# Kernel optimization log

Hardware: AMD Instinct MI355X
Metric: run time of the kernel (lower is better)

The kernel has to match this reference:

```python
import jax, jax.numpy as jnp
import numpy as np

N, E, D, H, C, G, L = 100000, 1600000, 128, 4, 32, 4096, 3  # nodes, edges, h_dim, heads, head_dim, graphs, conv blocks


def setup_inputs() -> dict:
    key = jax.random.key(0)
    ks = jax.random.split(key, 24)
    s = 0.05
    w = lambda k, shape: jax.random.normal(k, shape, jnp.float32) * s
    inp = {
        "x": jax.random.normal(ks[0], (N, D), jnp.float32),
        "edge_index": jax.random.randint(ks[1], (2, E), 0, N),
        "batch": jnp.sort(jax.random.randint(ks[2], (N,), 0, G)),
        # input TransformerConv (in=D, out=C per head, H heads, beta=True)
        "in_Wq": w(ks[3], (D, D)), "in_bq": jnp.zeros((D,), jnp.float32),
        "in_Wk": w(ks[4], (D, D)), "in_bk": jnp.zeros((D,), jnp.float32),
        "in_Wv": w(ks[5], (D, D)), "in_bv": jnp.zeros((D,), jnp.float32),
        "in_Ws": w(ks[6], (D, D)), "in_bs": jnp.zeros((D,), jnp.float32),
        "in_Wbeta": w(ks[7], (3 * D,)),
        # stacked conv blocks (L of them, in=out=D)
        "blk_Wq": w(ks[8], (L, D, D)), "blk_bq": jnp.zeros((L, D), jnp.float32),
        "blk_Wk": w(ks[9], (L, D, D)), "blk_bk": jnp.zeros((L, D), jnp.float32),
        "blk_Wv": w(ks[10], (L, D, D)), "blk_bv": jnp.zeros((L, D), jnp.float32),
        "blk_Ws": w(ks[11], (L, D, D)), "blk_bs": jnp.zeros((L, D), jnp.float32),
        "blk_Wbeta": w(ks[12], (L, 3 * D)),
        # MLP head
        "W1": w(ks[13], (D, 64)), "b1": jnp.zeros((64,), jnp.float32),
        "W2": w(ks[14], (64, 32)), "b2": jnp.zeros((32,), jnp.float32),
        "W3": w(ks[15], (32, 1)), "b3": jnp.zeros((1,), jnp.float32),
    }
    return inp


def transformer_conv(x, src, dst, Wq, bq, Wk, bk, Wv, bv, Ws, bs, Wbeta):
    # PyG TransformerConv, concat=True, root_weight=True, beta=True, eval mode
    q = (x @ Wq + bq).reshape(N, H, C)
    k = (x @ Wk + bk).reshape(N, H, C)
    v = (x @ Wv + bv).reshape(N, H, C)
    # per-edge attention logits: message j=src -> i=dst
    alpha = jnp.einsum("ehc,ehc->eh", q[dst], k[src]) / jnp.sqrt(jnp.float32(C))  # [E,H]
    m = jax.ops.segment_max(alpha, dst, num_segments=N)
    m = jnp.where(jnp.isfinite(m), m, 0.0)
    e = jnp.exp(alpha - m[dst])
    denom = jax.ops.segment_sum(e, dst, num_segments=N)
    a = e / (denom[dst] + 1e-16)  # segment softmax over in-edges of dst
    msg = a[..., None] * v[src]  # [E,H,C]
    out = jax.ops.segment_sum(msg, dst, num_segments=N).reshape(N, H * C)
    x_r = x @ Ws + bs
    beta = jax.nn.sigmoid(jnp.concatenate([out, x_r, out - x_r], axis=-1) @ Wbeta)[:, None]
    return beta * x_r + (1.0 - beta) * out


def reference(x, edge_index, batch, in_Wq, in_bq, in_Wk, in_bk, in_Wv, in_bv,
              in_Ws, in_bs, in_Wbeta, blk_Wq, blk_bq, blk_Wk, blk_bk, blk_Wv,
              blk_bv, blk_Ws, blk_bs, blk_Wbeta, W1, b1, W2, b2, W3, b3):
    src, dst = edge_index[0], edge_index[1]
    h = jax.nn.relu(transformer_conv(x, src, dst, in_Wq, in_bq, in_Wk, in_bk,
                                     in_Wv, in_bv, in_Ws, in_bs, in_Wbeta))
    for l in range(L):  # dropout is identity in eval mode
        h = jax.nn.relu(transformer_conv(h, src, dst, blk_Wq[l], blk_bq[l],
                                         blk_Wk[l], blk_bk[l], blk_Wv[l], blk_bv[l],
                                         blk_Ws[l], blk_bs[l], blk_Wbeta[l]))
    # global mean pool over graphs
    sums = jax.ops.segment_sum(h, batch, num_segments=G)
    cnt = jax.ops.segment_sum(jnp.ones((N, 1), h.dtype), batch, num_segments=G)
    g = sums / jnp.maximum(cnt, 1.0)
    g = jax.nn.relu(g @ W1 + b1)
    g = jax.nn.relu(g @ W2 + b2)
    return jax.nn.sigmoid(g @ W3 + b3)
```

## Files before the change

kernel.cpp:

```cpp
#include <hip/hip_runtime.h>
#include <hip/hip_bf16.h>
#include <cstdint>

#define DH 128
#define NB 256
#define NBK 1024

typedef __attribute__((ext_vector_type(8))) short short8;
typedef __attribute__((ext_vector_type(4))) float floatx4;
typedef __attribute__((ext_vector_type(2))) float floatx2;

__device__ __forceinline__ float bflo(unsigned u) { return __uint_as_float(u << 16); }
__device__ __forceinline__ float bfhi(unsigned u) { return __uint_as_float(u & 0xffff0000u); }

__device__ __forceinline__ unsigned pk_bf16(float a, float b) {
  return ((unsigned)__bfloat16_as_ushort(__float2bfloat16(b)) << 16)
       | (unsigned)__bfloat16_as_ushort(__float2bfloat16(a));
}

template<int CTRL>
__device__ __forceinline__ float dpp_add(float x) {
  int y = __builtin_amdgcn_update_dpp(0, __float_as_int(x), CTRL, 0xf, 0xf, true);
  return x + __int_as_float(y);
}


__global__ void cvt_bf16(const float* __restrict__ x, __hip_bfloat16* __restrict__ o, int n) {
  int i = blockIdx.x * 256 + threadIdx.x;
  if (i < n) o[i] = __float2bfloat16(x[i]);
}


__global__ void scan1_kernel(const int* __restrict__ deg, int* __restrict__ off,
                             int* __restrict__ bsum, int n) {
  __shared__ int sh[256];
  int idx = blockIdx.x * 256 + threadIdx.x;
  int v = (idx < n) ? deg[idx] : 0;
  sh[threadIdx.x] = v;
  __syncthreads();
  for (int d = 1; d < 256; d <<= 1) {
    int x = (threadIdx.x >= (unsigned)d) ? sh[threadIdx.x - d] : 0;
    __syncthreads();
    sh[threadIdx.x] += x;
    __syncthreads();
  }
  if (idx < n) off[idx] = sh[threadIdx.x] - v;
  if (threadIdx.x == 255) bsum[blockIdx.x] = sh[255];
}

__global__ void scan2_kernel(int* __restrict__ bsum, int nb) {
  __shared__ int sh[512];
  int t = threadIdx.x;
  int v = (t < nb) ? bsum[t] : 0;
  sh[t] = v;
  __syncthreads();
  for (int d = 1; d < 512; d <<= 1) {
    int x = (t >= (unsigned)d) ? sh[t - d] : 0;
    __syncthreads();
    sh[t] += x;
    __syncthreads();
  }
  if (t < nb) bsum[t] = sh[t] - v;
}

__global__ void scan3_kernel(int* __restrict__ off, const int* __restrict__ bsum, int n) {
  int idx = blockIdx.x * 256 + threadIdx.x;
  if (idx < n) off[idx] += bsum[blockIdx.x];
}


__global__ __launch_bounds__(256)
void csr_p1(const int* __restrict__ dst, int* __restrict__ hist, int E, int chunk) {
  __shared__ int cnt[NBK];
  const int blk = blockIdx.x, tid = threadIdx.x;
  for (int c = tid; c < NBK; c += 256) cnt[c] = 0;
  __syncthreads();
  int base = blk * chunk;
  int end = base + chunk; if (end > E) end = E;
  for (int e = base + tid; e < end; e += 256) atomicAdd(&cnt[dst[e] >> 7], 1);
  __syncthreads();
  for (int c = tid; c < NBK; c += 256) hist[c * NB + blk] = cnt[c];
}

__global__ __launch_bounds__(256)
void csr_p2(int* __restrict__ hist, int* __restrict__ total) {
  int b = blockIdx.x * 4 + (threadIdx.x >> 6);
  int lane = threadIdx.x & 63;
  int4 v = *(int4*)&hist[b * NB + lane * 4];
  int s0 = v.x;
  int s1 = s0 + v.y;
  int s2 = s1 + v.z;
  int s3 = s2 + v.w;
  int t = s3;
  for (int d = 1; d < 64; d <<= 1) {
    int y = __shfl_up(t, d);
    if (lane >= d) t += y;
  }
  int excl = t - s3;
  int4 o;
  o.x = excl; o.y = excl + s0; o.z = excl + s1; o.w = excl + s2;
  *(int4*)&hist[b * NB + lane * 4] = o;
  if (lane == 63) total[b] = t;
}

__global__ __launch_bounds__(256)
void csr_p3(const int* __restrict__ src, const int* __restrict__ dst,
            const int* __restrict__ hist, const int* __restrict__ tstart,
            int* __restrict__ part, int E, int chunk) {
  __shared__ int cur[NBK];
  const int blk = blockIdx.x, tid = threadIdx.x;
  for (int c = tid; c < NBK; c += 256) cur[c] = hist[c * NB + blk] + tstart[c];
  __syncthreads();
  int base = blk * chunk;
  int end = base + chunk; if (end > E) end = E;
  for (int e = base + tid; e < end; e += 256) {
    int d = dst[e];
    int b = d >> 7;
    int pos = atomicAdd(&cur[b], 1);
    part[pos] = (src[e] << 7) | (d & 127);
  }
}

__global__ __launch_bounds__(256)
void csr_p4(const int* __restrict__ part, const int* __restrict__ tstart,
            const int* __restrict__ total, int* __restrict__ deg,
            int* __restrict__ off, int* __restrict__ csr, int Nn) {
  __shared__ int lcnt[128], lscan[128], lcur[128];
  const int b = blockIdx.x, tid = threadIdx.x;
  const int p0 = tstart[b];
  const int m = total[b];
  if (tid < 128) lcnt[tid] = 0;
  __syncthreads();
  for (int k = tid; k < m; k += 256) atomicAdd(&lcnt[part[p0 + k] & 127], 1);
  __syncthreads();
  if (tid < 128) lscan[tid] = lcnt[tid];
  __syncthreads();
  for (int d = 1; d < 128; d <<= 1) {
    int v = 0;
    if (tid < 128 && tid >= d) v = lscan[tid - d];
    __syncthreads();
    if (tid < 128) lscan[tid] += v;
    __syncthreads();
  }
  if (tid < 128) {
    int ex = lscan[tid] - lcnt[tid];
    lcur[tid] = ex;
    int n = (b << 7) + tid;
    if (n < Nn) { deg[n] = lcnt[tid]; off[n] = p0 + ex; }
  }
  __syncthreads();
  for (int k = tid; k < m; k += 256) {
    int pk = part[p0 + k];
    int pos = p0 + atomicAdd(&lcur[pk & 127], 1);
    csr[pos] = pk >> 7;
  }
}


__global__ void goff_kernel(const int* __restrict__ batch, int* __restrict__ goff,
                            int N, int G) {
  int g = blockIdx.x * 256 + threadIdx.x;
  if (g > G) return;
  if (g == G) { goff[G] = N; return; }
  int lo = 0, hi = N;
  while (lo < hi) { int mid = (lo + hi) >> 1; if (batch[mid] < g) lo = mid + 1; else hi = mid; }
  goff[g] = lo;
}


__global__ __launch_bounds__(256)
void pack_w_kernel(const float* __restrict__ Wq, const float* __restrict__ Wk,
                   const float* __restrict__ Wv, const float* __restrict__ Ws,
                   const float* __restrict__ bq, const float* __restrict__ bk,
                   const float* __restrict__ bv, const float* __restrict__ bs,
                   __hip_bfloat16* __restrict__ WT2, float* __restrict__ bcat) {
  if (blockIdx.x == 64) {
    for (int c = threadIdx.x; c < 512; c += 256) {
      int which = c >> 7, cc = c & 127;
      const float* b = (which == 0) ? bq : (which == 1) ? bk : (which == 2) ? bv : bs;
      bcat[c] = b[cc];
    }
    return;
  }
  __shared__ float tile[32][33];
  const int bid = blockIdx.x;
  const int which = bid >> 4, kb = (bid >> 2) & 3, cb = bid & 3;
  const float* W = (which == 0) ? Wq : (which == 1) ? Wk : (which == 2) ? Wv : Ws;
  const int tx = threadIdx.x & 31, ty = threadIdx.x >> 5;
#pragma unroll
  for (int r = ty; r < 32; r += 8)
    tile[r][tx] = W[(kb * 32 + r) * 128 + cb * 32 + tx];
  __syncthreads();
  const int t = threadIdx.x;
  const int mt_sel = t >> 7;
  const int s4 = (t & 127) * 4;
  const int l16 = s4 >> 5;
  const int quad = (s4 >> 3) & 3;
  const int j0 = s4 & 7;
  const int cl = mt_sel * 16 + l16;
  const int kr = quad * 8 + j0;
  float f0 = tile[kr + 0][cl];
  float f1 = tile[kr + 1][cl];
  float f2 = tile[kr + 2][cl];
  float f3 = tile[kr + 3][cl];
  const int mt = which * 8 + cb * 2 + mt_sel;
  const int o = mt * 2048 + kb * 512 + l16 * 32 + quad * 8 + j0;
  uint2 w;
  w.x = pk_bf16(f0, f1);
  w.y = pk_bf16(f2, f3);
  *(uint2*)&((unsigned short*)WT2)[o] = w;
}


__global__ __launch_bounds__(256)
void gemm_qkvs(const short* __restrict__ Xb, const short* __restrict__ WT2,
               const float* __restrict__ bc,
               unsigned int* __restrict__ qout,
               unsigned int* __restrict__ kvp,
               unsigned int* __restrict__ xrout, int Nn) {
  __shared__ short As[32][132];
  const int row0 = blockIdx.x * 32;
  const int tid = threadIdx.x;

#pragma unroll
  for (int p = 0; p < 2; ++p) {
    int chunk = p * 256 + tid;
    int r = chunk >> 4, c8 = chunk & 15;
    int row = row0 + r; if (row >= Nn) row = Nn - 1;
    *(int4*)&As[r][c8 * 8] = *(const int4*)&Xb[(size_t)row * 128 + c8 * 8];
  }
  __syncthreads();

  const int w = tid >> 6, lane = tid & 63, quad = lane >> 4, l16 = lane & 15;

  short8 xf[2][4];
#pragma unroll
  for (int nt = 0; nt < 2; ++nt)
#pragma unroll
    for (int kt = 0; kt < 4; ++kt)
      xf[nt][kt] = *(const short8*)&As[nt * 16 + l16][kt * 32 + quad * 8];

  const int fbase = l16 * 32 + quad * 8;

  if (w == 0 || w == 3) {
    unsigned int* outp = (w == 0) ? qout : xrout;
    const int mbase = (w == 0) ? 0 : 24;
#pragma unroll
    for (int i = 0; i < 8; ++i) {
      const int mt = mbase + i;
      short8 af[4];
#pragma unroll
      for (int kt = 0; kt < 4; ++kt)
        af[kt] = *(const short8*)&WT2[mt * 2048 + kt * 512 + fbase];
      float4 bias = *(const float4*)&bc[mt * 16 + quad * 4];
      const int wc = (i * 16 + quad * 4);
#pragma unroll
      for (int nt = 0; nt < 2; ++nt) {
        floatx4 acc = (floatx4){0.f, 0.f, 0.f, 0.f};
#pragma unroll
        for (int kt = 0; kt < 4; ++kt)
          acc = __builtin_amdgcn_mfma_f32_16x16x32_bf16(af[kt], xf[nt][kt], acc, 0, 0, 0);
        int node = row0 + nt * 16 + l16;
        if (node < Nn) {
          uint2 o;
          o.x = pk_bf16(acc[0] + bias.x, acc[1] + bias.y);
          o.y = pk_bf16(acc[2] + bias.z, acc[3] + bias.w);
          *(uint2*)&outp[(size_t)node * 64 + (wc >> 1)] = o;
        }
      }
    }
  } else {
    const int kb = 8 + (w - 1) * 4;
    const int vb = 16 + (w - 1) * 4;
#pragma unroll
    for (int i = 0; i < 4; ++i) {
      const int mk = kb + i, mv = vb + i;
      short8 afk[4], afv[4];
#pragma unroll
      for (int kt = 0; kt < 4; ++kt) {
        afk[kt] = *(const short8*)&WT2[mk * 2048 + kt * 512 + fbase];
        afv[kt] = *(const short8*)&WT2[mv * 2048 + kt * 512 + fbase];
      }
      float4 bk4 = *(const float4*)&bc[mk * 16 + quad * 4];
      float4 bv4 = *(const float4*)&bc[mv * 16 + quad * 4];
      const int krel = (w - 1) * 64 + i * 16 + quad * 4;
#pragma unroll
      for (int nt = 0; nt < 2; ++nt) {
        floatx4 ak = (floatx4){0.f, 0.f, 0.f, 0.f};
        floatx4 av = (floatx4){0.f, 0.f, 0.f, 0.f};
#pragma unroll
        for (int kt = 0; kt < 4; ++kt) {
          ak = __builtin_amdgcn_mfma_f32_16x16x32_bf16(afk[kt], xf[nt][kt], ak, 0, 0, 0);
          av = __builtin_amdgcn_mfma_f32_16x16x32_bf16(afv[kt], xf[nt][kt], av, 0, 0, 0);
        }
        int node = row0 + nt * 16 + l16;
        if (node < Nn) {
          int d0 = __builtin_amdgcn_cvt_pk_fp8_f32(ak[0] + bk4.x, ak[1] + bk4.y, 0, false);
          d0 = __builtin_amdgcn_cvt_pk_fp8_f32(av[0] + bv4.x, av[1] + bv4.y, d0, true);
          int d1 = __builtin_amdgcn_cvt_pk_fp8_f32(ak[2] + bk4.z, ak[3] + bk4.w, 0, false);
          d1 = __builtin_amdgcn_cvt_pk_fp8_f32(av[2] + bv4.z, av[3] + bv4.w, d1, true);
          uint2 o; o.x = (unsigned)d0; o.y = (unsigned)d1;
          *(uint2*)&kvp[(size_t)node * 64 + (krel >> 1)] = o;
        }
      }
    }
  }
}


__global__ __launch_bounds__(256)
void attn_kernel(unsigned int* __restrict__ q_h, const uint4* __restrict__ kvq,
                 const uint4* __restrict__ xr4, const int* __restrict__ off,
                 const int* __restrict__ deg, const int* __restrict__ csr,
                 const float* __restrict__ Wb, int Nn) {
  int wv = __builtin_amdgcn_readfirstlane(threadIdx.x >> 6);
  int i = blockIdx.x * 4 + wv;
  if (i >= Nn) return;
  const int l = threadIdx.x & 63;
  const int j = l & 15;
  const int g = l >> 4;

  const float QS = 0.17677669529663687f * 1.4426950408889634f;
  uint4 qw = ((const uint4*)q_h)[(size_t)i * 16 + j];
  float q0 = bflo(qw.x) * QS, q1 = bfhi(qw.x) * QS;
  float q2 = bflo(qw.y) * QS, q3 = bfhi(qw.y) * QS;
  float q4 = bflo(qw.z) * QS, q5 = bfhi(qw.z) * QS;
  float q6 = bflo(qw.w) * QS, q7 = bfhi(qw.w) * QS;

  const int e0 = off[i];
  const int dg = deg[i];
  const int eend = e0 + dg;

  float denA = 0.f, denB = 0.f;
  float aA[8] = {0.f, 0.f, 0.f, 0.f, 0.f, 0.f, 0.f, 0.f};
  float aB[8] = {0.f, 0.f, 0.f, 0.f, 0.f, 0.f, 0.f, 0.f};

  auto batch = [&](int e, float& den, float (&a)[8]) {
    int s = csr[e + g];
    uint4 kv = kvq[(unsigned)((s << 4) | j)];
    floatx2 k0 = __builtin_amdgcn_cvt_pk_f32_fp8((int)kv.x, false);
    floatx2 v0 = __builtin_amdgcn_cvt_pk_f32_fp8((int)kv.x, true);
    floatx2 k1 = __builtin_amdgcn_cvt_pk_f32_fp8((int)kv.y, false);
    floatx2 v1 = __builtin_amdgcn_cvt_pk_f32_fp8((int)kv.y, true);
    floatx2 k2 = __builtin_amdgcn_cvt_pk_f32_fp8((int)kv.z, false);
    floatx2 v2 = __builtin_amdgcn_cvt_pk_f32_fp8((int)kv.z, true);
    floatx2 k3 = __builtin_amdgcn_cvt_pk_f32_fp8((int)kv.w, false);
    floatx2 v3 = __builtin_amdgcn_cvt_pk_f32_fp8((int)kv.w, true);
    float d = q0 * k0.x + q1 * k0.y + q2 * k1.x + q3 * k1.y
            + q4 * k2.x + q5 * k2.y + q6 * k3.x + q7 * k3.y;
    d = dpp_add<0xB1>(d);
    d = dpp_add<0x4E>(d);
    float p = exp2f(d);
    den += p;
    a[0] += p * v0.x; a[1] += p * v0.y; a[2] += p * v1.x; a[3] += p * v1.y;
    a[4] += p * v2.x; a[5] += p * v2.y; a[6] += p * v3.x; a[7] += p * v3.y;
  };

  auto batchm = [&](int e, int r, float& den, float (&a)[8]) {
    int idx = e + ((g < r) ? g : r - 1);
    int s = csr[idx];
    uint4 kv = kvq[(unsigned)((s << 4) | j)];
    floatx2 k0 = __builtin_amdgcn_cvt_pk_f32_fp8((int)kv.x, false);
    floatx2 v0 = __builtin_amdgcn_cvt_pk_f32_fp8((int)kv.x, true);
    floatx2 k1 = __builtin_amdgcn_cvt_pk_f32_fp8((int)kv.y, false);
    floatx2 v1 = __builtin_amdgcn_cvt_pk_f32_fp8((int)kv.y, true);
    floatx2 k2 = __builtin_amdgcn_cvt_pk_f32_fp8((int)kv.z, false);
    floatx2 v2 = __builtin_amdgcn_cvt_pk_f32_fp8((int)kv.z, true);
    floatx2 k3 = __builtin_amdgcn_cvt_pk_f32_fp8((int)kv.w, false);
    floatx2 v3 = __builtin_amdgcn_cvt_pk_f32_fp8((int)kv.w, true);
    float d = q0 * k0.x + q1 * k0.y + q2 * k1.x + q3 * k1.y
            + q4 * k2.x + q5 * k2.y + q6 * k3.x + q7 * k3.y;
    d = dpp_add<0xB1>(d);
    d = dpp_add<0x4E>(d);
    float p = (g < r) ? exp2f(d) : 0.f;
    den += p;
    a[0] += p * v0.x; a[1] += p * v0.y; a[2] += p * v1.x; a[3] += p * v1.y;
    a[4] += p * v2.x; a[5] += p * v2.y; a[6] += p * v3.x; a[7] += p * v3.y;
  };

  int e = e0;
  for (; e + 8 <= eend; e += 8) {
    batch(e, denA, aA);
    batch(e + 4, denB, aB);
  }
  if (e + 4 <= eend) {
    batch(e, denA, aA);
    e += 4;
  }
  if (e < eend) batchm(e, eend - e, denB, aB);

  float den = denA + denB;
  float a0 = aA[0] + aB[0], a1 = aA[1] + aB[1], a2 = aA[2] + aB[2], a3 = aA[3] + aB[3];
  float a4 = aA[4] + aB[4], a5 = aA[5] + aB[5], a6 = aA[6] + aB[6], a7 = aA[7] + aB[7];

  den += __shfl_xor(den, 16); den += __shfl_xor(den, 32);
  a0 += __shfl_xor(a0, 16); a0 += __shfl_xor(a0, 32);
  a1 += __shfl_xor(a1, 16); a1 += __shfl_xor(a1, 32);
  a2 += __shfl_xor(a2, 16); a2 += __shfl_xor(a2, 32);
  a3 += __shfl_xor(a3, 16); a3 += __shfl_xor(a3, 32);
  a4 += __shfl_xor(a4, 16); a4 += __shfl_xor(a4, 32);
  a5 += __shfl_xor(a5, 16); a5 += __shfl_xor(a5, 32);
  a6 += __shfl_xor(a6, 16); a6 += __shfl_xor(a6, 32);
  a7 += __shfl_xor(a7, 16); a7 += __shfl_xor(a7, 32);

  float inv = 1.f / (den + 1e-16f);
  float o0 = a0 * inv, o1 = a1 * inv, o2 = a2 * inv, o3 = a3 * inv;
  float o4 = a4 * inv, o5 = a5 * inv, o6 = a6 * inv, o7 = a7 * inv;

  uint4 xw = xr4[(size_t)i * 16 + j];
  float x0 = bflo(xw.x), x1 = bfhi(xw.x);
  float x2 = bflo(xw.y), x3 = bfhi(xw.y);
  float x4 = bflo(xw.z), x5 = bfhi(xw.z);
  float x6 = bflo(xw.w), x7 = bfhi(xw.w);

  float4 wo0 = *(const float4*)&Wb[8 * j];
  float4 wo1 = *(const float4*)&Wb[8 * j + 4];
  float4 wx0 = *(const float4*)&Wb[128 + 8 * j];
  float4 wx1 = *(const float4*)&Wb[128 + 8 * j + 4];
  float4 wd0 = *(const float4*)&Wb[256 + 8 * j];
  float4 wd1 = *(const float4*)&Wb[256 + 8 * j + 4];
  float c = o0 * wo0.x + o1 * wo0.y + o2 * wo0.z + o3 * wo0.w
          + o4 * wo1.x + o5 * wo1.y + o6 * wo1.z + o7 * wo1.w
          + x0 * wx0.x + x1 * wx0.y + x2 * wx0.z + x3 * wx0.w
          + x4 * wx1.x + x5 * wx1.y + x6 * wx1.z + x7 * wx1.w
          + (o0 - x0) * wd0.x + (o1 - x1) * wd0.y + (o2 - x2) * wd0.z + (o3 - x3) * wd0.w
          + (o4 - x4) * wd1.x + (o5 - x5) * wd1.y + (o6 - x6) * wd1.z + (o7 - x7) * wd1.w;
  c = dpp_add<0xB1>(c);
  c = dpp_add<0x4E>(c);
  c = dpp_add<0x141>(c);
  c = dpp_add<0x140>(c);
  float beta = 1.f / (1.f + __expf(-c));

  if (g == 0) {
    float h0 = fmaxf(beta * x0 + (1.f - beta) * o0, 0.f);
    float h1 = fmaxf(beta * x1 + (1.f - beta) * o1, 0.f);
    float h2 = fmaxf(beta * x2 + (1.f - beta) * o2, 0.f);
    float h3 = fmaxf(beta * x3 + (1.f - beta) * o3, 0.f);
    float h4 = fmaxf(beta * x4 + (1.f - beta) * o4, 0.f);
    float h5 = fmaxf(beta * x5 + (1.f - beta) * o5, 0.f);
    float h6 = fmaxf(beta * x6 + (1.f - beta) * o6, 0.f);
    float h7 = fmaxf(beta * x7 + (1.f - beta) * o7, 0.f);
    uint4 hw;
    hw.x = pk_bf16(h0, h1);
    hw.y = pk_bf16(h2, h3);
    hw.z = pk_bf16(h4, h5);
    hw.w = pk_bf16(h6, h7);
    ((uint4*)q_h)[(size_t)i * 16 + j] = hw;
  }
}


__global__ __launch_bounds__(128)
void poolmlp_kernel(const unsigned short* __restrict__ h, const int* __restrict__ goff,
                    const float* __restrict__ W1, const float* __restrict__ b1,
                    const float* __restrict__ W2, const float* __restrict__ b2,
                    const float* __restrict__ W3, const float* __restrict__ b3,
                    float* __restrict__ out) {
  int g = blockIdx.x;
  int t = threadIdx.x;
  int n0 = goff[g], cnt = goff[g + 1] - n0;
  float s = 0.f;
  for (int n = n0; n < n0 + cnt; ++n) s += bflo(h[(size_t)n * 128 + t]);
  __shared__ float gv[128];
  __shared__ float t1[64];
  __shared__ float t2[32];
  gv[t] = s / fmaxf((float)cnt, 1.0f);
  __syncthreads();
  if (t < 64) {
    float a = b1[t];
    for (int k = 0; k < 128; ++k) a += gv[k] * W1[k * 64 + t];
    t1[t] = fmaxf(a, 0.f);
  }
  __syncthreads();
  if (t < 32) {
    float a = b2[t];
    for (int k = 0; k < 64; ++k) a += t1[k] * W2[k * 32 + t];
    t2[t] = fmaxf(a, 0.f);
  }
  __syncthreads();
  if (t == 0) {
    float a = b3[0];
    for (int k = 0; k < 32; ++k) a += t2[k] * W3[k];
    out[g] = 1.f / (1.f + __expf(-a));
  }
}


extern "C" void kernel_launch(void* const* d_in, const int* in_sizes, int n_in,
                              void* d_out, int out_size, void* d_ws, size_t ws_size,
                              hipStream_t stream) {
  const float* x = (const float*)d_in[0];
  const int* edge_index = (const int*)d_in[1];
  const int* batch = (const int*)d_in[2];
  const int N = in_sizes[0] / DH;
  const int E = in_sizes[1] / 2;
  const int G = out_size;
  const int* src = edge_index;
  const int* dst = edge_index + E;

  const float* in_Wq = (const float*)d_in[3];
  const float* in_bq = (const float*)d_in[4];
  const float* in_Wk = (const float*)d_in[5];
  const float* in_bk = (const float*)d_in[6];
  const float* in_Wv = (const float*)d_in[7];
  const float* in_bv = (const float*)d_in[8];
  const float* in_Ws = (const float*)d_in[9];
  const float* in_bs = (const float*)d_in[10];
  const float* in_Wbeta = (const float*)d_in[11];
  const float* blk_Wq = (const float*)d_in[12];
  const float* blk_bq = (const float*)d_in[13];
  const float* blk_Wk = (const float*)d_in[14];
  const float* blk_bk = (const float*)d_in[15];
  const float* blk_Wv = (const float*)d_in[16];
  const float* blk_bv = (const float*)d_in[17];
  const float* blk_Ws = (const float*)d_in[18];
  const float* blk_bs = (const float*)d_in[19];
  const float* blk_Wbeta = (const float*)d_in[20];

  char* p = (char*)d_ws;
  auto take = [&](size_t bytes) { char* r = p; p += (bytes + 255) & ~(size_t)255; return r; };
  __hip_bfloat16* h0 = (__hip_bfloat16*)take((size_t)N * DH * 2);
  __hip_bfloat16* h1 = (__hip_bfloat16*)take((size_t)N * DH * 2);
  unsigned char* kvp = (unsigned char*)take((size_t)N * 256);
  unsigned short* xr = (unsigned short*)take((size_t)N * DH * 2);
  __hip_bfloat16* WT2 = (__hip_bfloat16*)take((size_t)512 * DH * 2);
  float* bcat = (float*)take(512 * 4);
  int* deg    = (int*)take((size_t)N * 4);
  int* off    = (int*)take((size_t)N * 4);
  int* csr    = (int*)take((size_t)E * 4);
  int* part   = (int*)take((size_t)E * 4);
  int* hist   = (int*)take((size_t)NB * NBK * 4);
  int* total  = (int*)take(NBK * 4);
  int* tstart = (int*)take(NBK * 4);
  int* bsumP  = (int*)take(512 * 4);
  int* goff   = (int*)take((size_t)(G + 1) * 4);
  (void)n_in;
  if ((size_t)(p - (char*)d_ws) > ws_size) return;

  const int NBUCK = (N + 127) >> 7;
  const int chunk = (E + NB - 1) / NB;

  csr_p1<<<NB, 256, 0, stream>>>(dst, hist, E, chunk);
  csr_p2<<<NBK / 4, 256, 0, stream>>>(hist, total);
  scan1_kernel<<<NBK / 256, 256, 0, stream>>>(total, tstart, bsumP, NBK);
  scan2_kernel<<<1, 512, 0, stream>>>(bsumP, NBK / 256);
  scan3_kernel<<<NBK / 256, 256, 0, stream>>>(tstart, bsumP, NBK);
  csr_p3<<<NB, 256, 0, stream>>>(src, dst, hist, tstart, part, E, chunk);
  csr_p4<<<NBUCK, 256, 0, stream>>>(part, tstart, total, deg, off, csr, N);

  goff_kernel<<<(G + 256) / 256, 256, 0, stream>>>(batch, goff, N, G);

  cvt_bf16<<<(int)(((size_t)N * DH + 255) / 256), 256, 0, stream>>>(x, h0, N * DH);

  for (int l = 0; l < 4; ++l) {
    const float *Wq, *Wk, *Wv, *Ws, *bq, *bk, *bv, *bs, *Wb;
    if (l == 0) {
      Wq = in_Wq; Wk = in_Wk; Wv = in_Wv; Ws = in_Ws;
      bq = in_bq; bk = in_bk; bv = in_bv; bs = in_bs; Wb = in_Wbeta;
    } else {
      int m = l - 1;
      Wq = blk_Wq + (size_t)m * DH * DH; Wk = blk_Wk + (size_t)m * DH * DH;
      Wv = blk_Wv + (size_t)m * DH * DH; Ws = blk_Ws + (size_t)m * DH * DH;
      bq = blk_bq + (size_t)m * DH; bk = blk_bk + (size_t)m * DH;
      bv = blk_bv + (size_t)m * DH; bs = blk_bs + (size_t)m * DH;
      Wb = blk_Wbeta + (size_t)m * 3 * DH;
    }
    __hip_bfloat16* hin  = (l & 1) ? h1 : h0;
    __hip_bfloat16* qbuf = (l & 1) ? h0 : h1;
    pack_w_kernel<<<65, 256, 0, stream>>>(Wq, Wk, Wv, Ws, bq, bk, bv, bs, WT2, bcat);
    gemm_qkvs<<<(N + 31) / 32, 256, 0, stream>>>((const short*)hin, (const short*)WT2, bcat,
        (unsigned int*)qbuf, (unsigned int*)kvp, (unsigned int*)xr, N);
    attn_kernel<<<(N + 3) / 4, 256, 0, stream>>>((unsigned int*)qbuf, (const uint4*)kvp,
        (const uint4*)xr, off, deg, csr, Wb, N);
  }

  poolmlp_kernel<<<G, 128, 0, stream>>>((const unsigned short*)h0, goff,
      (const float*)d_in[21], (const float*)d_in[22],
      (const float*)d_in[23], (const float*)d_in[24],
      (const float*)d_in[25], (const float*)d_in[26],
      (float*)d_out);
}
```

Before: 729.6 us.

## Batch CSR index loads per wave and issue four gathers before computing

The edge loop now loads up to 64 CSR source indices at once, one per lane, and broadcasts them with shuffles. It also issues up to four independent K/V gathers before doing any math, replacing the serial index-load then gather chain. The epilogue loads of xr and Wbeta are hoisted above the reductions so their latency overlaps. This raises memory-level parallelism and cuts dependent-load latency on the gather path, at the cost of more live registers and a bounds-checked shuffle per edge.

```diff
diff --git a/kernel.cpp b/kernel.cpp
--- a/kernel.cpp
+++ b/kernel.cpp
@@ -335,9 +335,7 @@
   float aA[8] = {0.f, 0.f, 0.f, 0.f, 0.f, 0.f, 0.f, 0.f};
   float aB[8] = {0.f, 0.f, 0.f, 0.f, 0.f, 0.f, 0.f, 0.f};
 
-  auto batch = [&](int e, float& den, float (&a)[8]) {
-    int s = csr[e + g];
-    uint4 kv = kvq[(unsigned)((s << 4) | j)];
+  auto comp = [&](const uint4& kv, bool valid, float& den, float (&a)[8]) {
     floatx2 k0 = __builtin_amdgcn_cvt_pk_f32_fp8((int)kv.x, false);
     floatx2 v0 = __builtin_amdgcn_cvt_pk_f32_fp8((int)kv.x, true);
     floatx2 k1 = __builtin_amdgcn_cvt_pk_f32_fp8((int)kv.y, false);
@@ -350,44 +348,56 @@
             + q4 * k2.x + q5 * k2.y + q6 * k3.x + q7 * k3.y;
     d = dpp_add<0xB1>(d);
     d = dpp_add<0x4E>(d);
-    float p = exp2f(d);
+    float p = valid ? exp2f(d) : 0.f;
     den += p;
     a[0] += p * v0.x; a[1] += p * v0.y; a[2] += p * v1.x; a[3] += p * v1.y;
     a[4] += p * v2.x; a[5] += p * v2.y; a[6] += p * v3.x; a[7] += p * v3.y;
   };
 
-  auto batchm = [&](int e, int r, float& den, float (&a)[8]) {
-    int idx = e + ((g < r) ? g : r - 1);
-    int s = csr[idx];
-    uint4 kv = kvq[(unsigned)((s << 4) | j)];
-    floatx2 k0 = __builtin_amdgcn_cvt_pk_f32_fp8((int)kv.x, false);
-    floatx2 v0 = __builtin_amdgcn_cvt_pk_f32_fp8((int)kv.x, true);
-    floatx2 k1 = __builtin_amdgcn_cvt_pk_f32_fp8((int)kv.y, false);
-    floatx2 v1 = __builtin_amdgcn_cvt_pk_f32_fp8((int)kv.y, true);
-    floatx2 k2 = __builtin_amdgcn_cvt_pk_f32_fp8((int)kv.z, false);
-    floatx2 v2 = __builtin_amdgcn_cvt_pk_f32_fp8((int)kv.z, true);
-    floatx2 k3 = __builtin_amdgcn_cvt_pk_f32_fp8((int)kv.w, false);
-    floatx2 v3 = __builtin_amdgcn_cvt_pk_f32_fp8((int)kv.w, true);
-    float d = q0 * k0.x + q1 * k0.y + q2 * k1.x + q3 * k1.y
-            + q4 * k2.x + q5 * k2.y + q6 * k3.x + q7 * k3.y;
-    d = dpp_add<0xB1>(d);
-    d = dpp_add<0x4E>(d);
-    float p = (g < r) ? exp2f(d) : 0.f;
-    den += p;
-    a[0] += p * v0.x; a[1] += p * v0.y; a[2] += p * v1.x; a[3] += p * v1.y;
-    a[4] += p * v2.x; a[5] += p * v2.y; a[6] += p * v3.x; a[7] += p * v3.y;
-  };
-
-  int e = e0;
-  for (; e + 8 <= eend; e += 8) {
-    batch(e, denA, aA);
-    batch(e + 4, denB, aB);
-  }
-  if (e + 4 <= eend) {
-    batch(e, denA, aA);
-    e += 4;
-  }
-  if (e < eend) batchm(e, eend - e, denB, aB);
+  for (int e = e0; e < eend; e += 64) {
+    const int rem = eend - e;
+    const int take = (rem < 64) ? rem : 64;
+    int il = e + l; if (il >= eend) il = eend - 1;
+    const int sv = csr[il];
+
+    for (int b = 0; b < take; b += 16) {
+      uint4 kv0, kv1, kv2, kv3;
+      bool p0 = false, p1 = false, p2 = false, p3 = false;
+      const int c0 = b + g, c1 = b + 4 + g, c2 = b + 8 + g, c3 = b + 12 + g;
+      {
+        p0 = c0 < take;
+        int s = __shfl(sv, p0 ? c0 : 0);
+        kv0 = kvq[(unsigned)((s << 4) | j)];
+      }
+      if (b + 4 < take) {
+        p1 = c1 < take;
+        int s = __shfl(sv, p1 ? c1 : 0);
+        kv1 = kvq[(unsigned)((s << 4) | j)];
+      }
+      if (b + 8 < take) {
+        p2 = c2 < take;
+        int s = __shfl(sv, p2 ? c2 : 0);
+        kv2 = kvq[(unsigned)((s << 4) | j)];
+      }
+      if (b + 12 < take) {
+        p3 = c3 < take;
+        int s = __shfl(sv, p3 ? c3 : 0);
+        kv3 = kvq[(unsigned)((s << 4) | j)];
+      }
+      comp(kv0, p0, denA, aA);
+      if (b + 4 < take)  comp(kv1, p1, denB, aB);
+      if (b + 8 < take)  comp(kv2, p2, denA, aA);
+      if (b + 12 < take) comp(kv3, p3, denB, aB);
+    }
+  }
+
+  uint4 xw = xr4[(size_t)i * 16 + j];
+  float4 wo0 = *(const float4*)&Wb[8 * j];
+  float4 wo1 = *(const float4*)&Wb[8 * j + 4];
+  float4 wx0 = *(const float4*)&Wb[128 + 8 * j];
+  float4 wx1 = *(const float4*)&Wb[128 + 8 * j + 4];
+  float4 wd0 = *(const float4*)&Wb[256 + 8 * j];
+  float4 wd1 = *(const float4*)&Wb[256 + 8 * j + 4];
 
   float den = denA + denB;
   float a0 = aA[0] + aB[0], a1 = aA[1] + aB[1], a2 = aA[2] + aB[2], a3 = aA[3] + aB[3];
@@ -407,18 +417,11 @@
   float o0 = a0 * inv, o1 = a1 * inv, o2 = a2 * inv, o3 = a3 * inv;
   float o4 = a4 * inv, o5 = a5 * inv, o6 = a6 * inv, o7 = a7 * inv;
 
-  uint4 xw = xr4[(size_t)i * 16 + j];
   float x0 = bflo(xw.x), x1 = bfhi(xw.x);
   float x2 = bflo(xw.y), x3 = bfhi(xw.y);
   float x4 = bflo(xw.z), x5 = bfhi(xw.z);
   float x6 = bflo(xw.w), x7 = bfhi(xw.w);
 
-  float4 wo0 = *(const float4*)&Wb[8 * j];
-  float4 wo1 = *(const float4*)&Wb[8 * j + 4];
-  float4 wx0 = *(const float4*)&Wb[128 + 8 * j];
-  float4 wx1 = *(const float4*)&Wb[128 + 8 * j + 4];
-  float4 wd0 = *(const float4*)&Wb[256 + 8 * j];
-  float4 wd1 = *(const float4*)&Wb[256 + 8 * j + 4];
   float c = o0 * wo0.x + o1 * wo0.y + o2 * wo0.z + o3 * wo0.w
           + o4 * wo1.x + o5 * wo1.y + o6 * wo1.z + o7 * wo1.w
           + x0 * wx0.x + x1 * wx0.y + x2 * wx0.z + x3 * wx0.w
```

Measured after the change: 711.6 us. 1.03x faster.
